# Performance work log

Hardware: AMD Instinct MI355X
Metric: run time of the kernel (lower is better)

Reference implementation:

```python
import jax, jax.numpy as jnp
import numpy as np

NUM_WIRES = 14
N_LAYERS = 4
BATCH = 128


def _rx_mat(theta):
    # PennyLane RX(t) = [[cos(t/2), -i sin(t/2)], [-i sin(t/2), cos(t/2)]]
    c = jnp.cos(theta / 2).astype(jnp.complex64)
    s = jnp.sin(theta / 2).astype(jnp.complex64)
    row0 = jnp.stack([c, -1j * s], axis=-1)
    row1 = jnp.stack([-1j * s, c], axis=-1)
    return jnp.stack([row0, row1], axis=-2)  # (..., 2, 2)


def _rz_mat(theta):
    # PennyLane RZ(t) = diag(exp(-it/2), exp(it/2))
    e0 = jnp.exp(-1j * theta.astype(jnp.complex64) / 2)
    e1 = jnp.exp(1j * theta.astype(jnp.complex64) / 2)
    z = jnp.zeros_like(e0)
    row0 = jnp.stack([e0, z], axis=-1)
    row1 = jnp.stack([z, e1], axis=-1)
    return jnp.stack([row0, row1], axis=-2)


def _apply_1q(psi, gate, wire):
    # psi: (B, 2, 2, ..., 2); gate: (2,2) shared or (B,2,2) per-sample
    axis = wire + 1
    psi = jnp.moveaxis(psi, axis, -1)
    if gate.ndim == 2:
        psi = psi @ gate.T
    else:
        psi = jnp.einsum('b...j,bij->b...i', psi, gate)
    return jnp.moveaxis(psi, -1, axis)


def _apply_cnot(psi, ctrl, tgt):
    ac, at = ctrl + 1, tgt + 1
    psi0 = jnp.take(psi, 0, axis=ac)
    psi1 = jnp.take(psi, 1, axis=ac)
    at_adj = at - (1 if at > ac else 0)  # target axis shifts after removing ctrl axis
    psi1 = jnp.flip(psi1, axis=at_adj)   # X on target when ctrl=1
    return jnp.stack([psi0, psi1], axis=ac)


def _circuit(x, weights):
    # x: (B, n) real angles; weights: (L, n, 2)
    B = x.shape[0]
    n = NUM_WIRES
    psi = jnp.zeros((B,) + (2,) * n, jnp.complex64)
    psi = psi.at[(slice(None),) + (0,) * n].set(1.0)  # |0...0>
    # data encoding: per-sample RX gates
    for i in range(n):
        psi = _apply_1q(psi, _rx_mat(x[:, i]), i)
    # variational ansatz
    for l in range(N_LAYERS):
        for i in range(n):
            psi = _apply_1q(psi, _rx_mat(weights[l, i, 0]), i)
            psi = _apply_1q(psi, _rz_mat(weights[l, i, 1]), i)
        for i in range(n - 1):
            psi = _apply_cnot(psi, i, i + 1)
        psi = _apply_cnot(psi, n - 1, 0)
    # <Z_i> for every wire
    p = jnp.abs(psi) ** 2  # (B, 2, ..., 2) real
    zs = []
    for i in range(n):
        other = tuple(a for a in range(1, n + 1) if a != i + 1)
        m = jnp.sum(p, axis=other)  # (B, 2)
        zs.append(m[:, 0] - m[:, 1])
    return jnp.stack(zs, axis=-1)  # (B, n)


def setup_inputs() -> dict:
    key = jax.random.key(0)
    k1, k2, k3, k4 = jax.random.split(key, 4)
    states = jax.random.normal(k1, (BATCH, 2 ** NUM_WIRES), dtype=jnp.float32)
    weights = jax.random.normal(k2, (N_LAYERS, NUM_WIRES, 2), dtype=jnp.float32)
    lim = 1.0 / np.sqrt(NUM_WIRES)
    head_w = jax.random.uniform(k3, (1, NUM_WIRES), jnp.float32, -lim, lim)
    head_b = jax.random.uniform(k4, (1,), jnp.float32, -lim, lim)
    return {"states": states, "weights": weights, "head_w": head_w, "head_b": head_b}


def reference(states, weights, head_w, head_b):
    features = jnp.abs(states)[:, :NUM_WIRES]        # (B, n)
    qfeatures = _circuit(features, weights)          # (B, n)
    out = (qfeatures @ head_w.T + head_b)[:, 0]      # (B,)
    return out
```

## Files before the change

### kernel.cpp

```cpp
#include <hip/hip_runtime.h>
#include <math.h>

#define NW 14
#define NSTATE 16384
#define HALF 8192
#define NL 4
#define BATCH 128
#define TPB 1024
#define SHB1 (84 * 1024)


#define B12_ 0x3FFFu
#define B13_ 0x1FFFu

#define WAVE_FENCE() __builtin_amdgcn_wave_barrier()

__device__ __forceinline__ unsigned sxmap(unsigned v) {
    unsigned t = v;
    t ^= t >> 1; t ^= t >> 2; t ^= t >> 4; t ^= t >> 8;
    return (t & 0x0FFFu) | ((t & 1u) << 13);
}

__device__ __forceinline__ float2 cmul(float2 u, float2 v) {
    return make_float2(u.x * v.x - u.y * v.y, u.x * v.y + u.y * v.x);
}

__device__ __forceinline__ float4 fused_coef(const float* weights,
                                             const float* states,
                                             int b, int l, int w) {
    float t1 = weights[(l * NW + w) * 2 + 0];
    float t2 = weights[(l * NW + w) * 2 + 1];
    if (l == 0) t1 += fabsf(states[(size_t)b * NSTATE + w]);
    float s, c, sz, cz;
    sincosf(0.5f * t1, &s, &c);
    sincosf(0.5f * t2, &sz, &cz);
    return make_float4(c * cz, -c * sz, -s * sz, -s * cz);
}

template<int N, int M>
__device__ __forceinline__ void gateN(float2* r, float4 g, unsigned s3) {
    const float f = (s3 & (unsigned)M) ? -1.0f : 1.0f;
    g.y *= f;
    g.z *= f;
#pragma unroll
    for (int k = 0; k < N; ++k) {
        if ((k & M) == 0) {
            const float x0 = r[k].x,   y0 = r[k].y;
            const float x1 = r[k|M].x, y1 = r[k|M].y;
            r[k].x   =  g.x*x0 - g.y*y0 + g.z*x1 - g.w*y1;
            r[k].y   =  g.x*y0 + g.y*x0 + g.z*y1 + g.w*x1;
            r[k|M].x = -g.z*x0 - g.w*y0 + g.x*x1 + g.y*y1;
            r[k|M].y = -g.z*y0 + g.w*x0 + g.x*y1 - g.y*x1;
        }
    }
}

template<int J0, int S3SH, int S3MSK>
__device__ __forceinline__ void pass3h(float2* psi, const float4* gc,
                                       unsigned t) {
    const float4 gA = gc[13 - (J0 + 0)];
    const float4 gB = gc[13 - (J0 + 1)];
    const float4 gC = gc[13 - (J0 + 2)];
    const unsigned s3   = (t >> S3SH) & (unsigned)S3MSK;
    const unsigned low  = t & ((1u << J0) - 1u);
    const unsigned high = (t >> J0) << (J0 + 3);
    float2 r[8];
#pragma unroll
    for (int k = 0; k < 8; ++k)
        r[k] = psi[low | (((unsigned)k ^ s3) << J0) | high];
    gateN<8,1>(r, gA, s3);
    gateN<8,2>(r, gB, s3);
    gateN<8,4>(r, gC, s3);
#pragma unroll
    for (int k = 0; k < 8; ++k)
        psi[low | (((unsigned)k ^ s3) << J0) | high] = r[k];
}

__device__ __forceinline__ void exit_scatter(const float2* psi,
                                             float2* __restrict__ dst,
                                             float4 g1, unsigned q,
                                             unsigned tid) {
#pragma unroll
    for (int m = 0; m < 4; ++m) {
        const unsigned jc = tid + (unsigned)m * TPB;
        const float2 x0 = psi[jc];
        const float2 x1 = psi[jc | 0x1000u];
        float2 A0, A1;
        A0.x =  g1.x*x0.x - g1.y*x0.y + g1.z*x1.x - g1.w*x1.y;
        A0.y =  g1.x*x0.y + g1.y*x0.x + g1.z*x1.y + g1.w*x1.x;
        A1.x = -g1.z*x0.x - g1.w*x0.y + g1.x*x1.x + g1.y*x1.y;
        A1.y = -g1.z*x0.y + g1.w*x0.x + g1.x*x1.y - g1.y*x1.x;
        const unsigned d0 = sxmap(jc) ^ (q ? 0x1FFFu : 0u);
        dst[d0]           = A0;
        dst[d0 ^ 0x3FFFu] = A1;
    }
}

__global__ __launch_bounds__(TPB) void k_layer1(
    const float* __restrict__ states, const float* __restrict__ weights,
    float2* __restrict__ Sout)
{
    extern __shared__ float2 psi[];
    __shared__ float2 vfac[NW][2];
    __shared__ float2 T1[128];
    __shared__ float2 T2[128];
    __shared__ float4 gc[NW];
    const unsigned gid = blockIdx.x, q = gid >> 7, b = gid & 127u;
    const unsigned tid = threadIdx.x;

    if (tid < NW) {
        float4 g = fused_coef(weights, states, (int)b, 0, (int)tid);
        vfac[tid][0] = make_float2(g.x, g.y);
        vfac[tid][1] = make_float2(-g.z, g.w);
    }
    if (tid >= 64 && tid < 64 + NW)
        gc[tid - 64] = fused_coef(weights, states, (int)b, 1, (int)(tid - 64));
    __syncthreads();
    if (tid < 128) {
        float2 p = make_float2(1.0f, 0.0f);
#pragma unroll
        for (int j = 0; j < 7; ++j)
            p = cmul(p, vfac[13 - j][(tid >> j) & 1u]);
        T1[tid] = p;
    } else if (tid < 256) {
        const unsigned u = tid - 128;
        float2 p = make_float2(1.0f, 0.0f);
#pragma unroll
        for (int j = 7; j < 14; ++j)
            p = cmul(p, vfac[13 - j][(u >> (j - 7)) & 1u]);
        T2[u] = p;
    }
    __syncthreads();

#pragma unroll
    for (int m = 0; m < 8; ++m) {
        const unsigned I  = tid + (unsigned)m * TPB;
        const unsigned If = I | (q << 13);
        const unsigned lo  = (If ^ (If >> 1)) & 0x0FFFu;
        const unsigned y12 = ((If >> 12) ^ (If >> 13) ^ If) & 1u;
        const unsigned y13 = ((If >> 13) ^ If) & 1u;
        const unsigned J = lo | (y12 << 12) | (y13 << 13);
        psi[I] = cmul(T1[J & 127u], T2[J >> 7]);
    }
    __syncthreads();

    pass3h<0, 1, 7>(psi, gc, tid);  WAVE_FENCE();
    pass3h<3, 3, 1>(psi, gc, tid);  WAVE_FENCE();
    pass3h<6, 0, 0>(psi, gc, tid);  __syncthreads();
    pass3h<9, 0, 0>(psi, gc, tid);  __syncthreads();

    exit_scatter(psi, Sout + (size_t)b * NSTATE, gc[1], q, tid);
}

__global__ __launch_bounds__(TPB) void k_mid(
    const float* __restrict__ states, const float* __restrict__ weights,
    const float* __restrict__ head_b,
    const float2* __restrict__ Sin, float2* __restrict__ Sout,
    float* __restrict__ out)
{
    extern __shared__ float2 psi[];
    __shared__ float4 gcx[NW + 1];
    const unsigned gid = blockIdx.x, q = gid >> 7, b = gid & 127u;
    const unsigned tid = threadIdx.x;

    if (tid < NW) gcx[tid] = fused_coef(weights, states, (int)b, 2, (int)tid);
    if (tid == 64) gcx[NW] = fused_coef(weights, states, (int)b, 1, 0);
    if (q == 0 && tid == 96) out[b] = head_b[0];
    __syncthreads();

    {
        const float4 ge = gcx[NW];
        const float2* src = Sin + (size_t)b * NSTATE + (size_t)q * HALF;
#pragma unroll
        for (int m = 0; m < 4; ++m) {
            const unsigned ic = tid + (unsigned)m * TPB;
            const float2 f0 = src[ic];
            const float2 f1 = src[ic ^ 0x1FFFu];
            const unsigned rc = (q ^ ic) & 1u;
            const float aar = ge.x, aai = rc ? -ge.y : ge.y;
            const float bbr = rc ? -ge.z : ge.z, bbi = ge.w;
            float2 oc, op;
            oc.x = aar*f0.x - aai*f0.y + bbr*f1.x - bbi*f1.y;
            oc.y = aar*f0.y + aai*f0.x + bbr*f1.y + bbi*f1.x;
            op.x = aar*f1.x + aai*f1.y - (bbr*f0.x + bbi*f0.y);
            op.y = aar*f1.y - aai*f1.x - (bbr*f0.y - bbi*f0.x);
            psi[ic]           = oc;
            psi[ic ^ 0x1FFFu] = op;
        }
    }
    __syncthreads();

    pass3h<0, 1, 7>(psi, gcx, tid);  WAVE_FENCE();
    pass3h<3, 3, 1>(psi, gcx, tid);  WAVE_FENCE();
    pass3h<6, 0, 0>(psi, gcx, tid);  __syncthreads();
    pass3h<9, 0, 0>(psi, gcx, tid);  __syncthreads();

    exit_scatter(psi, Sout + (size_t)b * NSTATE, gcx[1], q, tid);
}

__global__ __launch_bounds__(TPB) void k_last(
    const float* __restrict__ states, const float* __restrict__ weights,
    const float* __restrict__ head_w,
    const float2* __restrict__ Sin, float* __restrict__ out)
{
    extern __shared__ float2 psi[];
    __shared__ float4 gcx[NW + 1];
    __shared__ float wsum[TPB / 64];
    const unsigned gid = blockIdx.x, h = gid >> 7, b = gid & 127u;
    const unsigned tid = threadIdx.x;

    if (tid < NW) gcx[tid] = fused_coef(weights, states, (int)b, 3, (int)tid);
    if (tid == 64) gcx[NW] = fused_coef(weights, states, (int)b, 2, 0);
    __syncthreads();

    {
        const float4 ge = gcx[NW];
        const float4 g0 = gcx[0];
        const float ar = h ? -g0.z : g0.x;
        const float ai = h ?  g0.w : g0.y;
        const float br = h ?  g0.x : g0.z;
        const float bi = h ? -g0.y : g0.w;
        const float2* s0 = Sin + (size_t)b * NSTATE;
        const float2* s1 = s0 + HALF;
#pragma unroll
        for (int m = 0; m < 4; ++m) {
            const unsigned ic = tid + (unsigned)m * TPB;
            const unsigned jc = ic ^ 0x1FFFu;
            const float2 f00 = s0[ic], f01 = s0[jc];
            const float2 f10 = s1[ic], f11 = s1[jc];
            const unsigned rc = ic & 1u;
            float2 oc0, op0, oc1, op1;
            {
                const float aar = ge.x, aai = rc ? -ge.y : ge.y;
                const float bbr = rc ? -ge.z : ge.z, bbi = ge.w;
                oc0.x = aar*f00.x - aai*f00.y + bbr*f01.x - bbi*f01.y;
                oc0.y = aar*f00.y + aai*f00.x + bbr*f01.y + bbi*f01.x;
                op0.x = aar*f01.x + aai*f01.y - (bbr*f00.x + bbi*f00.y);
                op0.y = aar*f01.y - aai*f01.x - (bbr*f00.y - bbi*f00.x);
            }
            {
                const unsigned rx = rc ^ 1u;
                const float aar = ge.x, aai = rx ? -ge.y : ge.y;
                const float bbr = rx ? -ge.z : ge.z, bbi = ge.w;
                oc1.x = aar*f10.x - aai*f10.y + bbr*f11.x - bbi*f11.y;
                oc1.y = aar*f10.y + aai*f10.x + bbr*f11.y + bbi*f11.x;
                op1.x = aar*f11.x + aai*f11.y - (bbr*f10.x + bbi*f10.y);
                op1.y = aar*f11.y - aai*f11.x - (bbr*f10.y - bbi*f10.x);
            }
            float2 oA, oB;
            oA.x = ar*oc0.x - ai*oc0.y + br*oc1.x - bi*oc1.y;
            oA.y = ar*oc0.y + ai*oc0.x + br*oc1.y + bi*oc1.x;
            oB.x = ar*op0.x - ai*op0.y + br*op1.x - bi*op1.y;
            oB.y = ar*op0.y + ai*op0.x + br*op1.y + bi*op1.x;
            psi[ic] = oA;
            psi[jc] = oB;
        }
    }
    __syncthreads();

    pass3h<0, 1, 7>(psi, gcx, tid);  WAVE_FENCE();
    pass3h<3, 3, 1>(psi, gcx, tid);  WAVE_FENCE();
    pass3h<6, 0, 0>(psi, gcx, tid);  __syncthreads();
    pass3h<9, 0, 0>(psi, gcx, tid);  __syncthreads();

    float hw[NW];
#pragma unroll
    for (int i = 0; i < NW; ++i) hw[i] = head_w[i];
    float H = 0.0f, H12 = 0.0f;
#pragma unroll
    for (int i = 0; i < NW; ++i) H += hw[i];
#pragma unroll
    for (int i = 2; i < NW; ++i) H12 += hw[i];

    const float4 g1 = gcx[1];
    float acc = 0.0f;
#pragma unroll
    for (int m2 = 0; m2 < 4; ++m2) {
        const unsigned base = tid | ((unsigned)m2 << 10);
        float2 r[2];
        r[0] = psi[base];
        r[1] = psi[base | 0x1000u];
        gateN<2,1>(r, g1, 0u);
        float A = 0.0f;
        unsigned sfx = 0u;
#pragma unroll
        for (int p = 11; p >= 0; --p) {
            sfx ^= (base >> p) & 1u;
            if (sfx) A += hw[13 - p];
        }
        const unsigned P = sfx;
#pragma unroll
        for (int kk = 0; kk < 2; ++kk) {
            const unsigned u   = (unsigned)kk ^ h;
            const unsigned b13 = P ^ (unsigned)kk;
            float sum = u ? (H12 - A) : A;
            if (u)   sum += hw[1];
            if (b13) sum += hw[0];
            const float cv = H - 2.0f * sum;
            acc += (r[kk].x * r[kk].x + r[kk].y * r[kk].y) * cv;
        }
    }
#pragma unroll
    for (int off = 32; off > 0; off >>= 1)
        acc += __shfl_down(acc, off, 64);
    if ((tid & 63u) == 0) wsum[tid >> 6] = acc;
    __syncthreads();
    if (tid == 0) {
        float tot = 0.0f;
#pragma unroll
        for (int i = 0; i < TPB / 64; ++i) tot += wsum[i];
        atomicAdd(out + b, tot);
    }
}

extern "C" void kernel_launch(void* const* d_in, const int* in_sizes, int n_in,
                              void* d_out, int out_size, void* d_ws, size_t ws_size,
                              hipStream_t stream) {
    const float* states  = (const float*)d_in[0];
    const float* weights = (const float*)d_in[1];
    const float* head_w  = (const float*)d_in[2];
    const float* head_b  = (const float*)d_in[3];
    float* out = (float*)d_out;

    float2* SA = (float2*)d_ws;
    float2* SB = SA + (size_t)BATCH * NSTATE;

    k_layer1<<<2 * BATCH, TPB, SHB1, stream>>>(states, weights, SA);
    k_mid   <<<2 * BATCH, TPB, SHB1, stream>>>(states, weights, head_b,
                                               SA, SB, out);
    k_last  <<<2 * BATCH, TPB, SHB1, stream>>>(states, weights, head_w,
                                               SB, out);
}
```

Before: 108.1 us.

## Fuse three layer kernels into one with per-batch pairwise global flag sync

Merges the layer1, mid and last kernels into a single kernel. The two blocks handling each batch element synchronise through a global atomic counter between stages instead of at kernel boundaries. This is meant to remove inter-kernel launch gaps and tail effects. It relies on both blocks of a pair being co-resident, which risks deadlock, and it adds a memset to reset the flags.

```diff
diff --git a/kernel.cpp b/kernel.cpp
--- a/kernel.cpp
+++ b/kernel.cpp
@@ -96,15 +96,33 @@
     }
 }
 
-__global__ __launch_bounds__(TPB) void k_layer1(
+__device__ __forceinline__ void pair_sync(unsigned* flag, unsigned target,
+                                          unsigned tid) {
+    __syncthreads();
+    if (tid == 0) {
+        __threadfence();
+        __hip_atomic_fetch_add(flag, 1u, __ATOMIC_RELEASE,
+                               __HIP_MEMORY_SCOPE_AGENT);
+        while (__hip_atomic_load(flag, __ATOMIC_ACQUIRE,
+                                 __HIP_MEMORY_SCOPE_AGENT) < target)
+            __builtin_amdgcn_s_sleep(1);
+        __threadfence();
+    }
+    __syncthreads();
+}
+
+__global__ __launch_bounds__(TPB) void k_fused(
     const float* __restrict__ states, const float* __restrict__ weights,
-    float2* __restrict__ Sout)
+    const float* __restrict__ head_w, const float* __restrict__ head_b,
+    float2* __restrict__ SA, float2* __restrict__ SB,
+    unsigned* __restrict__ flags, float* __restrict__ out)
 {
     extern __shared__ float2 psi[];
     __shared__ float2 vfac[NW][2];
     __shared__ float2 T1[128];
     __shared__ float2 T2[128];
-    __shared__ float4 gc[NW];
+    __shared__ float4 gcx[NW + 1];
+    __shared__ float wsum[TPB / 64];
     const unsigned gid = blockIdx.x, q = gid >> 7, b = gid & 127u;
     const unsigned tid = threadIdx.x;
 
@@ -114,7 +132,8 @@
         vfac[tid][1] = make_float2(-g.z, g.w);
     }
     if (tid >= 64 && tid < 64 + NW)
-        gc[tid - 64] = fused_coef(weights, states, (int)b, 1, (int)(tid - 64));
+        gcx[tid - 64] = fused_coef(weights, states, (int)b, 1, (int)(tid - 64));
+    if (q == 0 && tid == 96) out[b] = head_b[0];
     __syncthreads();
     if (tid < 128) {
         float2 p = make_float2(1.0f, 0.0f);
@@ -144,33 +163,22 @@
     }
     __syncthreads();
 
-    pass3h<0, 1, 7>(psi, gc, tid);  WAVE_FENCE();
-    pass3h<3, 3, 1>(psi, gc, tid);  WAVE_FENCE();
-    pass3h<6, 0, 0>(psi, gc, tid);  __syncthreads();
-    pass3h<9, 0, 0>(psi, gc, tid);  __syncthreads();
-
-    exit_scatter(psi, Sout + (size_t)b * NSTATE, gc[1], q, tid);
-}
-
-__global__ __launch_bounds__(TPB) void k_mid(
-    const float* __restrict__ states, const float* __restrict__ weights,
-    const float* __restrict__ head_b,
-    const float2* __restrict__ Sin, float2* __restrict__ Sout,
-    float* __restrict__ out)
-{
-    extern __shared__ float2 psi[];
-    __shared__ float4 gcx[NW + 1];
-    const unsigned gid = blockIdx.x, q = gid >> 7, b = gid & 127u;
-    const unsigned tid = threadIdx.x;
+    pass3h<0, 1, 7>(psi, gcx, tid);  WAVE_FENCE();
+    pass3h<3, 3, 1>(psi, gcx, tid);  WAVE_FENCE();
+    pass3h<6, 0, 0>(psi, gcx, tid);  __syncthreads();
+    pass3h<9, 0, 0>(psi, gcx, tid);  __syncthreads();
+
+    exit_scatter(psi, SA + (size_t)b * NSTATE, gcx[1], q, tid);
+
+    pair_sync(flags + b, 2u, tid);
 
     if (tid < NW) gcx[tid] = fused_coef(weights, states, (int)b, 2, (int)tid);
     if (tid == 64) gcx[NW] = fused_coef(weights, states, (int)b, 1, 0);
-    if (q == 0 && tid == 96) out[b] = head_b[0];
     __syncthreads();
 
     {
         const float4 ge = gcx[NW];
-        const float2* src = Sin + (size_t)b * NSTATE + (size_t)q * HALF;
+        const float2* src = SA + (size_t)b * NSTATE + (size_t)q * HALF;
 #pragma unroll
         for (int m = 0; m < 4; ++m) {
             const unsigned ic = tid + (unsigned)m * TPB;
@@ -195,20 +203,11 @@
     pass3h<6, 0, 0>(psi, gcx, tid);  __syncthreads();
     pass3h<9, 0, 0>(psi, gcx, tid);  __syncthreads();
 
-    exit_scatter(psi, Sout + (size_t)b * NSTATE, gcx[1], q, tid);
-}
-
-__global__ __launch_bounds__(TPB) void k_last(
-    const float* __restrict__ states, const float* __restrict__ weights,
-    const float* __restrict__ head_w,
-    const float2* __restrict__ Sin, float* __restrict__ out)
-{
-    extern __shared__ float2 psi[];
-    __shared__ float4 gcx[NW + 1];
-    __shared__ float wsum[TPB / 64];
-    const unsigned gid = blockIdx.x, h = gid >> 7, b = gid & 127u;
-    const unsigned tid = threadIdx.x;
-
+    exit_scatter(psi, SB + (size_t)b * NSTATE, gcx[1], q, tid);
+
+    pair_sync(flags + b, 4u, tid);
+
+    const unsigned h = q;
     if (tid < NW) gcx[tid] = fused_coef(weights, states, (int)b, 3, (int)tid);
     if (tid == 64) gcx[NW] = fused_coef(weights, states, (int)b, 2, 0);
     __syncthreads();
@@ -220,7 +219,7 @@
         const float ai = h ?  g0.w : g0.y;
         const float br = h ?  g0.x : g0.z;
         const float bi = h ? -g0.y : g0.w;
-        const float2* s0 = Sin + (size_t)b * NSTATE;
+        const float2* s0 = SB + (size_t)b * NSTATE;
         const float2* s1 = s0 + HALF;
 #pragma unroll
         for (int m = 0; m < 4; ++m) {
@@ -324,10 +323,9 @@
 
     float2* SA = (float2*)d_ws;
     float2* SB = SA + (size_t)BATCH * NSTATE;
-
-    k_layer1<<<2 * BATCH, TPB, SHB1, stream>>>(states, weights, SA);
-    k_mid   <<<2 * BATCH, TPB, SHB1, stream>>>(states, weights, head_b,
-                                               SA, SB, out);
-    k_last  <<<2 * BATCH, TPB, SHB1, stream>>>(states, weights, head_w,
-                                               SB, out);
-}
+    unsigned* flags = (unsigned*)(SB + (size_t)BATCH * NSTATE);
+
+    hipMemsetAsync(flags, 0, BATCH * sizeof(unsigned), stream);
+    k_fused<<<2 * BATCH, TPB, SHB1, stream>>>(states, weights, head_w, head_b,
+                                              SA, SB, flags, out);
+}
```

After: 159.4 us. +47.5%, slower.
